# Optimization experiments

Hardware: AMD Instinct MI355X
Metric: run time of the kernel (lower is better)

## Reference

```python
import jax, jax.numpy as jnp
import numpy as np

N_NODES = 50000
N_EDGES = 800000
N_GRAPHS = 128
IN_C, HID_C, OUT_C = 128, 256, 128


def setup_inputs() -> dict:
    key = jax.random.key(0)
    ks = jax.random.split(key, 10)
    x = jax.random.normal(ks[0], (N_NODES, IN_C), dtype=jnp.float32)
    edge_index = jax.random.randint(ks[1], (2, N_EDGES), 0, N_NODES, dtype=jnp.int32)
    batch = jnp.sort(jax.random.randint(ks[2], (N_NODES,), 0, N_GRAPHS, dtype=jnp.int32))
    def glorot(k, fan_in, fan_out):
        lim = (6.0 / (fan_in + fan_out)) ** 0.5
        return jax.random.uniform(k, (fan_in, fan_out), jnp.float32, -lim, lim)
    W1 = glorot(ks[3], IN_C, HID_C)
    b1 = jnp.zeros((HID_C,), jnp.float32)
    W2 = glorot(ks[4], HID_C, HID_C)
    b2 = jnp.zeros((HID_C,), jnp.float32)
    Wfc = glorot(ks[5], HID_C, OUT_C)
    bfc = jnp.zeros((OUT_C,), jnp.float32)
    return {"x": x, "edge_index": edge_index, "batch": batch,
            "W1": W1, "b1": b1, "W2": W2, "b2": b2, "Wfc": Wfc, "bfc": bfc}


def _gcn_conv(x, src, dst, W, b, n_nodes):
    # PyG GCNConv: h = x @ W; out[dst] += norm * h[src]; out += b
    h = x @ W  # [N, F_out]
    ones = jnp.ones(src.shape, dtype=h.dtype)
    deg = jax.ops.segment_sum(ones, dst, num_segments=n_nodes)  # in-degree incl self loops
    dinv = jnp.where(deg > 0, jax.lax.rsqrt(deg), 0.0)
    norm = dinv[src] * dinv[dst]                    # [E]
    msg = h[src] * norm[:, None]                    # gather + scale, [E, F_out]
    out = jax.ops.segment_sum(msg, dst, num_segments=n_nodes)  # scatter-add
    return out + b


def reference(x, edge_index, batch, W1, b1, W2, b2, Wfc, bfc):
    n = x.shape[0]
    loops = jnp.arange(n, dtype=edge_index.dtype)
    src = jnp.concatenate([edge_index[0], loops])   # add self loops (GCNConv default)
    dst = jnp.concatenate([edge_index[1], loops])
    h = jax.nn.relu(_gcn_conv(x, src, dst, W1, b1, n))
    h = jax.nn.relu(_gcn_conv(h, src, dst, W2, b2, n))
    # global_mean_pool keyed by batch index
    sums = jax.ops.segment_sum(h, batch, num_segments=N_GRAPHS)          # [G, HID]
    cnts = jax.ops.segment_sum(jnp.ones((n,), h.dtype), batch, num_segments=N_GRAPHS)
    pooled = sums / jnp.maximum(cnts, 1.0)[:, None]
    return pooled @ Wfc + bfc
```

## Files before the change

kernel.cpp:

```cpp
#include <hip/hip_runtime.h>
#include <type_traits>

#define HID 256
#define INC 128
#define OUTC 128

typedef __attribute__((ext_vector_type(8))) short short8;
typedef __attribute__((ext_vector_type(4))) float floatx4;

__device__ __forceinline__ unsigned short f2bf(float f) {
    unsigned int u = __float_as_uint(f);
    unsigned int r = (u + 0x7FFFu + ((u >> 16) & 1u)) >> 16;
    return (unsigned short)r;
}

__device__ __forceinline__ void bfacc2(float* a, uint u, float nr) {
    a[0] = fmaf(nr, __uint_as_float(u << 16), a[0]);
    a[1] = fmaf(nr, __uint_as_float(u & 0xFFFF0000u), a[1]);
}

__global__ void k_convX(const float* __restrict__ x, unsigned short* __restrict__ xb, int total4) {
    int i = blockIdx.x * 256 + threadIdx.x;
    if (i < total4) {
        const float4 v = *(const float4*)(x + (size_t)i * 4);
        uint2 o;
        o.x = (unsigned)f2bf(v.x) | ((unsigned)f2bf(v.y) << 16);
        o.y = (unsigned)f2bf(v.z) | ((unsigned)f2bf(v.w) << 16);
        *(uint2*)(xb + (size_t)i * 4) = o;
    }
}

__global__ void k_hist(const int* __restrict__ dst, int* __restrict__ cnt, int e) {
    int i = blockIdx.x * blockDim.x + threadIdx.x;
    if (i < e) atomicAdd(&cnt[dst[i]], 1);
}

__global__ __launch_bounds__(256) void k_scan_local(const int* __restrict__ cnt,
                                                    int* __restrict__ ex, int* __restrict__ blk_sum,
                                                    float* __restrict__ dinv, int n) {
    __shared__ int s[256];
    const int t = threadIdx.x;
    const int i = blockIdx.x * 256 + t;
    const int v = (i < n) ? cnt[i] : 0;
    if (i < n) dinv[i] = rsqrtf((float)v + 1.0f);
    s[t] = v;
    __syncthreads();
    for (int off = 1; off < 256; off <<= 1) {
        int add = (t >= off) ? s[t - off] : 0;
        __syncthreads();
        s[t] += add;
        __syncthreads();
    }
    if (i < n) ex[i] = s[t] - v;
    if (t == 255) blk_sum[blockIdx.x] = s[255];
}

__global__ __launch_bounds__(256) void k_scan_add(int* __restrict__ row_ptr,
                                                  const int* __restrict__ blk_sum,
                                                  int* __restrict__ cnt, int n, int e) {
    __shared__ int s[256];
    const int t = threadIdx.x;
    const int b = blockIdx.x;
    s[t] = (t < b) ? blk_sum[t] : 0;
    __syncthreads();
    for (int off = 128; off > 0; off >>= 1) {
        if (t < off) s[t] += s[t + off];
        __syncthreads();
    }
    const int offset = s[0];
    const int i = b * 256 + t;
    if (i < n) { row_ptr[i] += offset; cnt[i] = 0; }
    if (i == 0) row_ptr[n] = e;
}

__global__ void k_fill(const int* __restrict__ src, const int* __restrict__ dst,
                       const int* __restrict__ row_ptr, int* __restrict__ cursor,
                       int* __restrict__ csr_src, int e) {
    int i = blockIdx.x * blockDim.x + threadIdx.x;
    if (i < e) {
        const int d = dst[i];
        const int pos = row_ptr[d] + atomicAdd(&cursor[d], 1);
        csr_src[pos] = src[i];
    }
}

__global__ void k_convW(const float* __restrict__ W1, unsigned short* __restrict__ Wt1,
                        const float* __restrict__ W2, unsigned short* __restrict__ Wt2) {
    int id = blockIdx.x * 256 + threadIdx.x;
    if (id < INC * HID) {
        int n = id / INC;
        int k = id - n * INC;
        Wt1[id] = f2bf(W1[k * HID + n]);
    } else if (id < INC * HID + HID * HID) {
        int id2 = id - INC * HID;
        int n = id2 / HID;
        int k = id2 - n * HID;
        Wt2[id2] = f2bf(W2[k * HID + n]);
    }
}

template <int CH>
__global__ __launch_bounds__(256) void k_agg(const unsigned short* __restrict__ h,
                                             const int* __restrict__ row_ptr,
                                             const int* __restrict__ csr_src,
                                             const float* __restrict__ dinv,
                                             unsigned short* __restrict__ out, int n) {
    constexpr int CPL = CH / 64;
    using VT = std::conditional_t<CPL == 2, uint, uint2>;
    const int v = (blockIdx.x * 256 + threadIdx.x) >> 6;
    const int lane = threadIdx.x & 63;
    if (v >= n) return;
    const float dv = dinv[v];
    const unsigned short* hl = h + lane * CPL;

    float acc[CPL];
    {
        const VT u = *(const VT*)(hl + (size_t)v * CH);
        const float s2 = dv * dv;
        if constexpr (CPL == 2) {
            acc[0] = s2 * __uint_as_float(((uint)u) << 16);
            acc[1] = s2 * __uint_as_float(((uint)u) & 0xFFFF0000u);
        } else {
            const uint2 w = (uint2)u;
            acc[0] = s2 * __uint_as_float(w.x << 16);
            acc[1] = s2 * __uint_as_float(w.x & 0xFFFF0000u);
            acc[2] = s2 * __uint_as_float(w.y << 16);
            acc[3] = s2 * __uint_as_float(w.y & 0xFFFF0000u);
        }
    }

    const int beg = row_ptr[v];
    const int end = row_ptr[v + 1];
    int i = beg;
    for (; i + 8 <= end; i += 8) {
        int si[8];
        float nr[8];
        VT r[8];
#pragma unroll
        for (int j = 0; j < 8; ++j) si[j] = csr_src[i + j];
#pragma unroll
        for (int j = 0; j < 8; ++j) nr[j] = dv * dinv[si[j]];
#pragma unroll
        for (int j = 0; j < 8; ++j) r[j] = *(const VT*)(hl + (size_t)si[j] * CH);
#pragma unroll
        for (int j = 0; j < 8; ++j) {
            if constexpr (CPL == 2) {
                bfacc2(acc, (uint)r[j], nr[j]);
            } else {
                const uint2 w = (uint2)r[j];
                bfacc2(acc, w.x, nr[j]);
                bfacc2(acc + 2, w.y, nr[j]);
            }
        }
    }
    for (; i < end; ++i) {
        const int s0 = csr_src[i];
        const float n0 = dv * dinv[s0];
        const VT r0 = *(const VT*)(hl + (size_t)s0 * CH);
        if constexpr (CPL == 2) {
            bfacc2(acc, (uint)r0, n0);
        } else {
            const uint2 w0 = (uint2)r0;
            bfacc2(acc, w0.x, n0); bfacc2(acc + 2, w0.y, n0);
        }
    }

    if constexpr (CPL == 2) {
        uint o = (unsigned)f2bf(acc[0]) | ((unsigned)f2bf(acc[1]) << 16);
        *(uint*)(out + (size_t)v * CH + lane * CPL) = o;
    } else {
        uint2 o;
        o.x = (unsigned)f2bf(acc[0]) | ((unsigned)f2bf(acc[1]) << 16);
        o.y = (unsigned)f2bf(acc[2]) | ((unsigned)f2bf(acc[3]) << 16);
        *(uint2*)(out + (size_t)v * CH + lane * CPL) = o;
    }
}

template <int K, bool RELU, bool POOL, typename OT>
__global__ __launch_bounds__(256) void k_gemm_mfma(const unsigned short* __restrict__ A,
                                                   const unsigned short* __restrict__ Wt,
                                                   const float* __restrict__ bias,
                                                   OT* __restrict__ out,
                                                   const int* __restrict__ batch,
                                                   float* __restrict__ pooled_sum, int M) {
    constexpr int LDA = K + 8;
    __shared__ unsigned short sA[32 * LDA];
    __shared__ int s_batch[32];
    const int t = threadIdx.x;
    const int row0 = blockIdx.x * 32;

    {
        const int r = t >> 3;
        const int c0 = (t & 7) * (K / 8);
        unsigned short* dstp = &sA[r * LDA + c0];
        if (row0 + r < M) {
            const unsigned short* srcp = A + (size_t)(row0 + r) * K + c0;
#pragma unroll
            for (int j = 0; j < K / 8; j += 8)
                *(uint4*)(dstp + j) = *(const uint4*)(srcp + j);
        } else {
            const uint4 z = {0, 0, 0, 0};
#pragma unroll
            for (int j = 0; j < K / 8; j += 8) *(uint4*)(dstp + j) = z;
        }
        if constexpr (POOL) {
            if (t < 32) s_batch[t] = (row0 + t < M) ? batch[row0 + t] : -1;
        }
    }
    __syncthreads();

    const int wv = t >> 6;
    const int lane = t & 63;
    const int m16 = lane & 15;
    const int quad = lane >> 4;

    floatx4 acc[2][4];
#pragma unroll
    for (int h2 = 0; h2 < 2; ++h2)
#pragma unroll
        for (int j = 0; j < 4; ++j) acc[h2][j] = (floatx4){0.f, 0.f, 0.f, 0.f};

    const unsigned short* ap0 = &sA[m16 * LDA + quad * 8];
    const unsigned short* ap1 = &sA[(16 + m16) * LDA + quad * 8];
    const unsigned short* bp = Wt + (size_t)(wv * 64 + m16) * K + quad * 8;

#pragma unroll
    for (int k0 = 0; k0 < K; k0 += 32) {
        const short8 a0 = *(const short8*)(ap0 + k0);
        const short8 a1 = *(const short8*)(ap1 + k0);
        const short8 b0 = *(const short8*)(bp + 0 * 16 * K + k0);
        const short8 b1 = *(const short8*)(bp + 1 * 16 * K + k0);
        const short8 b2 = *(const short8*)(bp + 2 * 16 * K + k0);
        const short8 b3 = *(const short8*)(bp + 3 * 16 * K + k0);
        acc[0][0] = __builtin_amdgcn_mfma_f32_16x16x32_bf16(a0, b0, acc[0][0], 0, 0, 0);
        acc[0][1] = __builtin_amdgcn_mfma_f32_16x16x32_bf16(a0, b1, acc[0][1], 0, 0, 0);
        acc[0][2] = __builtin_amdgcn_mfma_f32_16x16x32_bf16(a0, b2, acc[0][2], 0, 0, 0);
        acc[0][3] = __builtin_amdgcn_mfma_f32_16x16x32_bf16(a0, b3, acc[0][3], 0, 0, 0);
        acc[1][0] = __builtin_amdgcn_mfma_f32_16x16x32_bf16(a1, b0, acc[1][0], 0, 0, 0);
        acc[1][1] = __builtin_amdgcn_mfma_f32_16x16x32_bf16(a1, b1, acc[1][1], 0, 0, 0);
        acc[1][2] = __builtin_amdgcn_mfma_f32_16x16x32_bf16(a1, b2, acc[1][2], 0, 0, 0);
        acc[1][3] = __builtin_amdgcn_mfma_f32_16x16x32_bf16(a1, b3, acc[1][3], 0, 0, 0);
    }

    const int nbase = wv * 64 + m16;
    const float bb0 = bias[nbase + 0];
    const float bb1 = bias[nbase + 16];
    const float bb2 = bias[nbase + 32];
    const float bb3 = bias[nbase + 48];

    if constexpr (POOL) {
        float ps0 = 0.f, ps1 = 0.f, ps2 = 0.f, ps3 = 0.f;
        int gcur = -1;
#pragma unroll
        for (int h2 = 0; h2 < 2; ++h2) {
#pragma unroll
            for (int j = 0; j < 4; ++j) {
                const int rl = h2 * 16 + quad * 4 + j;
                const int g = s_batch[rl];
                if (g < 0) continue;
                if (g != gcur) {
                    if (gcur >= 0) {
                        float* pp = pooled_sum + gcur * HID + nbase;
                        atomicAdd(pp + 0, ps0);
                        atomicAdd(pp + 16, ps1);
                        atomicAdd(pp + 32, ps2);
                        atomicAdd(pp + 48, ps3);
                    }
                    ps0 = ps1 = ps2 = ps3 = 0.f;
                    gcur = g;
                }
                ps0 += fmaxf(acc[h2][0][j] + bb0, 0.f);
                ps1 += fmaxf(acc[h2][1][j] + bb1, 0.f);
                ps2 += fmaxf(acc[h2][2][j] + bb2, 0.f);
                ps3 += fmaxf(acc[h2][3][j] + bb3, 0.f);
            }
        }
        if (gcur >= 0) {
            float* pp = pooled_sum + gcur * HID + nbase;
            atomicAdd(pp + 0, ps0);
            atomicAdd(pp + 16, ps1);
            atomicAdd(pp + 32, ps2);
            atomicAdd(pp + 48, ps3);
        }
    } else {
#pragma unroll
        for (int h2 = 0; h2 < 2; ++h2) {
#pragma unroll
            for (int j = 0; j < 4; ++j) {
                const int row = row0 + h2 * 16 + quad * 4 + j;
                if (row >= M) continue;
                float v0 = acc[h2][0][j] + bb0;
                float v1 = acc[h2][1][j] + bb1;
                float v2 = acc[h2][2][j] + bb2;
                float v3 = acc[h2][3][j] + bb3;
                if constexpr (RELU) {
                    v0 = fmaxf(v0, 0.f); v1 = fmaxf(v1, 0.f);
                    v2 = fmaxf(v2, 0.f); v3 = fmaxf(v3, 0.f);
                }
                if constexpr (sizeof(OT) == 4) {
                    out[(size_t)row * HID + nbase + 0]  = v0;
                    out[(size_t)row * HID + nbase + 16] = v1;
                    out[(size_t)row * HID + nbase + 32] = v2;
                    out[(size_t)row * HID + nbase + 48] = v3;
                } else {
                    out[(size_t)row * HID + nbase + 0]  = f2bf(v0);
                    out[(size_t)row * HID + nbase + 16] = f2bf(v1);
                    out[(size_t)row * HID + nbase + 32] = f2bf(v2);
                    out[(size_t)row * HID + nbase + 48] = f2bf(v3);
                }
            }
        }
    }
}

__global__ void k_fc(const float* __restrict__ pooled_sum, const int* __restrict__ batch,
                     const float* __restrict__ W, const float* __restrict__ b,
                     float* __restrict__ out, int n) {
    const int g = blockIdx.x;
    const int c = threadIdx.x;
    int a = 0, hi = n;
    while (a < hi) { int m = (a + hi) >> 1; if (batch[m] < g) a = m + 1; else hi = m; }
    const int start = a;
    hi = n;
    while (a < hi) { int m = (a + hi) >> 1; if (batch[m] < g + 1) a = m + 1; else hi = m; }
    const float cnt = (float)(a - start);

    float acc = 0.0f;
    const float* p = pooled_sum + g * HID;
    for (int k = 0; k < HID; ++k) acc += p[k] * W[k * OUTC + c];
    out[g * OUTC + c] = acc / fmaxf(cnt, 1.0f) + b[c];
}

extern "C" void kernel_launch(void* const* d_in, const int* in_sizes, int n_in,
                              void* d_out, int out_size, void* d_ws, size_t ws_size,
                              hipStream_t stream) {
    const float* x   = (const float*)d_in[0];
    const int*   ei  = (const int*)d_in[1];
    const int*   bat = (const int*)d_in[2];
    const float* W1  = (const float*)d_in[3];
    const float* b1  = (const float*)d_in[4];
    const float* W2  = (const float*)d_in[5];
    const float* b2  = (const float*)d_in[6];
    const float* Wfc = (const float*)d_in[7];
    const float* bfc = (const float*)d_in[8];
    float* out = (float*)d_out;

    const int n = in_sizes[2];
    const int e = in_sizes[1] / 2;
    const int* src = ei;
    const int* dst = ei + e;
    const int nb = (n + 255) / 256;

    size_t off = 0;
    auto alloc = [&](size_t bytes) {
        char* p = (char*)d_ws + off;
        off += (bytes + 255) & ~(size_t)255;
        return p;
    };
    int*   cnt     = (int*)alloc((size_t)n * 4);
    int*   row_ptr = (int*)alloc((size_t)(n + 1) * 4);
    int*   blk_sum = (int*)alloc(512 * 4);
    int*   csr_src = (int*)alloc((size_t)e * 4);
    float* dinv    = (float*)alloc((size_t)n * 4);
    unsigned short* Wt1 = (unsigned short*)alloc((size_t)INC * HID * 2);
    unsigned short* Wt2 = (unsigned short*)alloc((size_t)HID * HID * 2);
    unsigned short* R1  = (unsigned short*)alloc((size_t)n * HID * 2);
    unsigned short* R2  = (unsigned short*)alloc((size_t)n * INC * 2);
    unsigned short* R3  = (unsigned short*)alloc((size_t)n * HID * 2);
    float* pooled = (float*)alloc((size_t)128 * HID * 4);

    const int TB = 256;
    hipMemsetAsync(cnt, 0, (size_t)n * 4, stream);
    hipMemsetAsync(pooled, 0, (size_t)128 * HID * 4, stream);

    k_convX<<<((n * INC / 4) + TB - 1) / TB, TB, 0, stream>>>(x, R1, n * INC / 4);

    k_hist<<<(e + TB - 1) / TB, TB, 0, stream>>>(dst, cnt, e);
    k_scan_local<<<nb, TB, 0, stream>>>(cnt, row_ptr, blk_sum, dinv, n);
    k_scan_add<<<nb, TB, 0, stream>>>(row_ptr, blk_sum, cnt, n, e);
    k_fill<<<(e + TB - 1) / TB, TB, 0, stream>>>(src, dst, row_ptr, cnt, csr_src, e);

    k_convW<<<(INC * HID + HID * HID + TB - 1) / TB, TB, 0, stream>>>(W1, Wt1, W2, Wt2);

    const int gemm_blocks = (n + 31) / 32;
    const int agg_blocks = (n + 3) / 4;

    k_agg<INC><<<agg_blocks, TB, 0, stream>>>(R1, row_ptr, csr_src, dinv, R2, n);
    k_gemm_mfma<INC, true, false, unsigned short><<<gemm_blocks, TB, 0, stream>>>(
        R2, Wt1, b1, R3, nullptr, nullptr, n);

    k_agg<HID><<<agg_blocks, TB, 0, stream>>>(R3, row_ptr, csr_src, dinv, R1, n);
    k_gemm_mfma<HID, true, true, float><<<gemm_blocks, TB, 0, stream>>>(
        R1, Wt2, b2, (float*)nullptr, bat, pooled, n);

    k_fc<<<128, 128, 0, stream>>>(pooled, bat, Wfc, bfc, out, n);
}
```

Baseline: 358.5 us.

## Store bf16 activations in 32-channel column slices for cache-local aggregation

Activations move from row-major to a sliced layout in which each 32-channel slice of all nodes is contiguous. The aggregation kernel now runs blocks per (slice, node chunk), and within a wavefront four edge subgroups each gather 64-byte rows before a shuffle reduction. Because each gathered slice covers only a fraction of the full feature array, the random neighbour gathers are meant to hit in L2/MALL. The cost is that each edge list is re-read once per slice, gathers become narrower, and the GEMM loads and stores now address the sliced layout.

```diff
diff --git a/kernel.cpp b/kernel.cpp
--- a/kernel.cpp
+++ b/kernel.cpp
@@ -1,5 +1,4 @@
 #include <hip/hip_runtime.h>
-#include <type_traits>
 
 #define HID 256
 #define INC 128
@@ -14,20 +13,23 @@
     return (unsigned short)r;
 }
 
-__device__ __forceinline__ void bfacc2(float* a, uint u, float nr) {
-    a[0] = fmaf(nr, __uint_as_float(u << 16), a[0]);
-    a[1] = fmaf(nr, __uint_as_float(u & 0xFFFF0000u), a[1]);
-}
-
-__global__ void k_convX(const float* __restrict__ x, unsigned short* __restrict__ xb, int total4) {
+__device__ __forceinline__ float bflo(uint u) { return __uint_as_float(u << 16); }
+__device__ __forceinline__ float bfhi(uint u) { return __uint_as_float(u & 0xFFFF0000u); }
+
+__device__ __forceinline__ size_t sl_addr(int v, int c, int n) {
+    return (size_t)(c >> 5) * ((size_t)n * 32) + (size_t)v * 32 + (c & 31);
+}
+
+__global__ void k_convX(const float* __restrict__ x, unsigned short* __restrict__ xb, int n) {
     int i = blockIdx.x * 256 + threadIdx.x;
-    if (i < total4) {
-        const float4 v = *(const float4*)(x + (size_t)i * 4);
-        uint2 o;
-        o.x = (unsigned)f2bf(v.x) | ((unsigned)f2bf(v.y) << 16);
-        o.y = (unsigned)f2bf(v.z) | ((unsigned)f2bf(v.w) << 16);
-        *(uint2*)(xb + (size_t)i * 4) = o;
-    }
+    if (i >= n * (INC / 4)) return;
+    const int v = i >> 5;
+    const int c0 = (i & 31) << 2;
+    const float4 f = *(const float4*)(x + (size_t)v * INC + c0);
+    uint2 o;
+    o.x = (unsigned)f2bf(f.x) | ((unsigned)f2bf(f.y) << 16);
+    o.y = (unsigned)f2bf(f.z) | ((unsigned)f2bf(f.w) << 16);
+    *(uint2*)(xb + sl_addr(v, c0, n)) = o;
 }
 
 __global__ void k_hist(const int* __restrict__ dst, int* __restrict__ cnt, int e) {
@@ -99,80 +101,67 @@
     }
 }
 
-template <int CH>
-__global__ __launch_bounds__(256) void k_agg(const unsigned short* __restrict__ h,
-                                             const int* __restrict__ row_ptr,
-                                             const int* __restrict__ csr_src,
-                                             const float* __restrict__ dinv,
-                                             unsigned short* __restrict__ out, int n) {
-    constexpr int CPL = CH / 64;
-    using VT = std::conditional_t<CPL == 2, uint, uint2>;
-    const int v = (blockIdx.x * 256 + threadIdx.x) >> 6;
+template <int CH, int NPB>
+__global__ __launch_bounds__(256) void k_agg_sl(const unsigned short* __restrict__ h,
+                                                const int* __restrict__ row_ptr,
+                                                const int* __restrict__ csr_src,
+                                                const float* __restrict__ dinv,
+                                                unsigned short* __restrict__ out, int n) {
+    constexpr int NSL = CH / 32;
+    const int slice = blockIdx.x % NSL;
+    const int chunk = blockIdx.x / NSL;
+    const int w = threadIdx.x >> 6;
     const int lane = threadIdx.x & 63;
-    if (v >= n) return;
-    const float dv = dinv[v];
-    const unsigned short* hl = h + lane * CPL;
-
-    float acc[CPL];
-    {
-        const VT u = *(const VT*)(hl + (size_t)v * CH);
-        const float s2 = dv * dv;
-        if constexpr (CPL == 2) {
-            acc[0] = s2 * __uint_as_float(((uint)u) << 16);
-            acc[1] = s2 * __uint_as_float(((uint)u) & 0xFFFF0000u);
-        } else {
-            const uint2 w = (uint2)u;
-            acc[0] = s2 * __uint_as_float(w.x << 16);
-            acc[1] = s2 * __uint_as_float(w.x & 0xFFFF0000u);
-            acc[2] = s2 * __uint_as_float(w.y << 16);
-            acc[3] = s2 * __uint_as_float(w.y & 0xFFFF0000u);
-        }
-    }
-
-    const int beg = row_ptr[v];
-    const int end = row_ptr[v + 1];
-    int i = beg;
-    for (; i + 8 <= end; i += 8) {
-        int si[8];
-        float nr[8];
-        VT r[8];
-#pragma unroll
-        for (int j = 0; j < 8; ++j) si[j] = csr_src[i + j];
-#pragma unroll
-        for (int j = 0; j < 8; ++j) nr[j] = dv * dinv[si[j]];
-#pragma unroll
-        for (int j = 0; j < 8; ++j) r[j] = *(const VT*)(hl + (size_t)si[j] * CH);
-#pragma unroll
-        for (int j = 0; j < 8; ++j) {
-            if constexpr (CPL == 2) {
-                bfacc2(acc, (uint)r[j], nr[j]);
-            } else {
-                const uint2 w = (uint2)r[j];
-                bfacc2(acc, w.x, nr[j]);
-                bfacc2(acc + 2, w.y, nr[j]);
-            }
-        }
-    }
-    for (; i < end; ++i) {
-        const int s0 = csr_src[i];
-        const float n0 = dv * dinv[s0];
-        const VT r0 = *(const VT*)(hl + (size_t)s0 * CH);
-        if constexpr (CPL == 2) {
-            bfacc2(acc, (uint)r0, n0);
-        } else {
-            const uint2 w0 = (uint2)r0;
-            bfacc2(acc, w0.x, n0); bfacc2(acc + 2, w0.y, n0);
-        }
-    }
-
-    if constexpr (CPL == 2) {
-        uint o = (unsigned)f2bf(acc[0]) | ((unsigned)f2bf(acc[1]) << 16);
-        *(uint*)(out + (size_t)v * CH + lane * CPL) = o;
-    } else {
-        uint2 o;
-        o.x = (unsigned)f2bf(acc[0]) | ((unsigned)f2bf(acc[1]) << 16);
-        o.y = (unsigned)f2bf(acc[2]) | ((unsigned)f2bf(acc[3]) << 16);
-        *(uint2*)(out + (size_t)v * CH + lane * CPL) = o;
+    const int esub = lane >> 4;
+    const int cl = lane & 15;
+
+    const unsigned short* hsl = h + (size_t)slice * n * 32 + cl * 2;
+    unsigned short* osl = out + (size_t)slice * n * 32 + cl * 2;
+
+    const int vend = min(chunk * NPB + NPB, n);
+    for (int v = chunk * NPB + w; v < vend; v += 4) {
+        const float dv = dinv[v];
+        const int beg = row_ptr[v];
+        const int end = row_ptr[v + 1];
+        float a0 = 0.f, a1 = 0.f;
+        int i = beg;
+        for (; i + 8 <= end; i += 8) {
+            const int s0 = csr_src[i + esub];
+            const int s1 = csr_src[i + 4 + esub];
+            const float n0 = dv * dinv[s0];
+            const float n1 = dv * dinv[s1];
+            const uint u0 = *(const uint*)(hsl + (size_t)s0 * 32);
+            const uint u1 = *(const uint*)(hsl + (size_t)s1 * 32);
+            a0 = fmaf(n0, bflo(u0), fmaf(n1, bflo(u1), a0));
+            a1 = fmaf(n0, bfhi(u0), fmaf(n1, bfhi(u1), a1));
+        }
+        if (i + 4 <= end) {
+            const int s0 = csr_src[i + esub];
+            const float n0 = dv * dinv[s0];
+            const uint u0 = *(const uint*)(hsl + (size_t)s0 * 32);
+            a0 = fmaf(n0, bflo(u0), a0);
+            a1 = fmaf(n0, bfhi(u0), a1);
+            i += 4;
+        }
+        if (i + esub < end) {
+            const int s0 = csr_src[i + esub];
+            const float n0 = dv * dinv[s0];
+            const uint u0 = *(const uint*)(hsl + (size_t)s0 * 32);
+            a0 = fmaf(n0, bflo(u0), a0);
+            a1 = fmaf(n0, bfhi(u0), a1);
+        }
+        a0 += __shfl_xor(a0, 16);
+        a0 += __shfl_xor(a0, 32);
+        a1 += __shfl_xor(a1, 16);
+        a1 += __shfl_xor(a1, 32);
+        if (esub == 0) {
+            const uint us = *(const uint*)(hsl + (size_t)v * 32);
+            const float s2 = dv * dv;
+            a0 = fmaf(s2, bflo(us), a0);
+            a1 = fmaf(s2, bfhi(us), a1);
+            const uint o = (unsigned)f2bf(a0) | ((unsigned)f2bf(a1) << 16);
+            *(uint*)(osl + (size_t)v * 32) = o;
+        }
     }
 }
 
@@ -191,13 +180,12 @@
 
     {
         const int r = t >> 3;
-        const int c0 = (t & 7) * (K / 8);
-        unsigned short* dstp = &sA[r * LDA + c0];
+        const int cbase = (t & 7) * (K / 8);
+        unsigned short* dstp = &sA[r * LDA + cbase];
         if (row0 + r < M) {
-            const unsigned short* srcp = A + (size_t)(row0 + r) * K + c0;
 #pragma unroll
             for (int j = 0; j < K / 8; j += 8)
-                *(uint4*)(dstp + j) = *(const uint4*)(srcp + j);
+                *(uint4*)(dstp + j) = *(const uint4*)(A + sl_addr(row0 + r, cbase + j, M));
         } else {
             const uint4 z = {0, 0, 0, 0};
 #pragma unroll
@@ -297,17 +285,10 @@
                     v0 = fmaxf(v0, 0.f); v1 = fmaxf(v1, 0.f);
                     v2 = fmaxf(v2, 0.f); v3 = fmaxf(v3, 0.f);
                 }
-                if constexpr (sizeof(OT) == 4) {
-                    out[(size_t)row * HID + nbase + 0]  = v0;
-                    out[(size_t)row * HID + nbase + 16] = v1;
-                    out[(size_t)row * HID + nbase + 32] = v2;
-                    out[(size_t)row * HID + nbase + 48] = v3;
-                } else {
-                    out[(size_t)row * HID + nbase + 0]  = f2bf(v0);
-                    out[(size_t)row * HID + nbase + 16] = f2bf(v1);
-                    out[(size_t)row * HID + nbase + 32] = f2bf(v2);
-                    out[(size_t)row * HID + nbase + 48] = f2bf(v3);
-                }
+                out[sl_addr(row, nbase + 0, M)]  = (OT)f2bf(v0);
+                out[sl_addr(row, nbase + 16, M)] = (OT)f2bf(v1);
+                out[sl_addr(row, nbase + 32, M)] = (OT)f2bf(v2);
+                out[sl_addr(row, nbase + 48, M)] = (OT)f2bf(v3);
             }
         }
     }
@@ -373,7 +354,7 @@
     hipMemsetAsync(cnt, 0, (size_t)n * 4, stream);
     hipMemsetAsync(pooled, 0, (size_t)128 * HID * 4, stream);
 
-    k_convX<<<((n * INC / 4) + TB - 1) / TB, TB, 0, stream>>>(x, R1, n * INC / 4);
+    k_convX<<<((n * INC / 4) + TB - 1) / TB, TB, 0, stream>>>(x, R1, n);
 
     k_hist<<<(e + TB - 1) / TB, TB, 0, stream>>>(dst, cnt, e);
     k_scan_local<<<nb, TB, 0, stream>>>(cnt, row_ptr, blk_sum, dinv, n);
@@ -383,13 +364,14 @@
     k_convW<<<(INC * HID + HID * HID + TB - 1) / TB, TB, 0, stream>>>(W1, Wt1, W2, Wt2);
 
     const int gemm_blocks = (n + 31) / 32;
-    const int agg_blocks = (n + 3) / 4;
-
-    k_agg<INC><<<agg_blocks, TB, 0, stream>>>(R1, row_ptr, csr_src, dinv, R2, n);
+    constexpr int NPB = 32;
+    const int chunks = (n + NPB - 1) / NPB;
+
+    k_agg_sl<INC, NPB><<<chunks * (INC / 32), TB, 0, stream>>>(R1, row_ptr, csr_src, dinv, R2, n);
     k_gemm_mfma<INC, true, false, unsigned short><<<gemm_blocks, TB, 0, stream>>>(
         R2, Wt1, b1, R3, nullptr, nullptr, n);
 
-    k_agg<HID><<<agg_blocks, TB, 0, stream>>>(R3, row_ptr, csr_src, dinv, R1, n);
+    k_agg_sl<HID, NPB><<<chunks * (HID / 32), TB, 0, stream>>>(R3, row_ptr, csr_src, dinv, R1, n);
     k_gemm_mfma<HID, true, true, float><<<gemm_blocks, TB, 0, stream>>>(
         R1, Wt2, b2, (float*)nullptr, bat, pooled, n);
 
```

New measurement: 455.0 us. +26.9%, slower.
